# Kernel optimization log

Hardware: AMD Instinct MI355X
Metric: run time of the kernel (lower is better)

The kernel has to match this reference:

```python
import jax, jax.numpy as jnp
import numpy as np

N_NODES = 100000
N_EDGES = 1600000
N_GRAPHS = 512
EPS = 1e-12


def _glorot(key, shape):
    lim = float(np.sqrt(6.0 / (shape[0] + shape[1])))
    return jax.random.uniform(key, shape, jnp.float32, -lim, lim)


def setup_inputs() -> dict:
    key = jax.random.key(0)
    ks = jax.random.split(key, 16)
    x = jax.random.normal(ks[0], (N_NODES, 5), jnp.float32)
    edge_index = jax.random.randint(ks[1], (2, N_EDGES), 0, N_NODES)
    batch = jnp.sort(jax.random.randint(ks[2], (N_NODES,), 0, N_GRAPHS))
    return {
        "x": x,
        "edge_index": edge_index,
        "batch": batch,
        "num_graphs": N_GRAPHS,
        # pre: Linear(5, 32)
        "pre_w": _glorot(ks[3], (5, 32)), "pre_b": jnp.zeros((32,), jnp.float32),
        # conv1: SAGEConv(32, 64): lin_l (agg, bias), lin_r (root, no bias)
        "c1_wl": _glorot(ks[4], (32, 64)), "c1_bl": jnp.zeros((64,), jnp.float32),
        "c1_wr": _glorot(ks[5], (32, 64)),
        # conv2: SAGEConv(64, 64)
        "c2_wl": _glorot(ks[6], (64, 64)), "c2_bl": jnp.zeros((64,), jnp.float32),
        "c2_wr": _glorot(ks[7], (64, 64)),
        # post / out linears
        "p1_w": _glorot(ks[8], (64, 64)), "p1_b": jnp.zeros((64,), jnp.float32),
        "p2_w": _glorot(ks[9], (64, 16)), "p2_b": jnp.zeros((16,), jnp.float32),
        "o_w": _glorot(ks[10], (16, 1)), "o_b": jnp.zeros((1,), jnp.float32),
    }


def _sage_conv(x, src, dst, w_l, b_l, w_r, n_nodes):
    # mean-aggregate neighbor messages src -> dst
    msg = x[src]                                              # [E, d]
    agg = jax.ops.segment_sum(msg, dst, num_segments=n_nodes)  # [N, d]
    cnt = jax.ops.segment_sum(jnp.ones((src.shape[0], 1), x.dtype), dst,
                              num_segments=n_nodes)            # [N, 1]
    agg = jnp.where(cnt > 0, agg / jnp.maximum(cnt, 1.0), 0.0)
    out = agg @ w_l + b_l + x @ w_r
    # normalize=True -> L2 normalize per node
    nrm = jnp.linalg.norm(out, axis=-1, keepdims=True)
    return out / jnp.maximum(nrm, EPS)


def reference(x, edge_index, batch, num_graphs,
              pre_w, pre_b, c1_wl, c1_bl, c1_wr, c2_wl, c2_bl, c2_wr,
              p1_w, p1_b, p2_w, p2_b, o_w, o_b):
    n_nodes = x.shape[0]
    src, dst = edge_index[0], edge_index[1]
    h = jax.nn.relu(x @ pre_w + pre_b)
    h = jax.nn.relu(_sage_conv(h, src, dst, c1_wl, c1_bl, c1_wr, n_nodes))
    h = jax.nn.relu(_sage_conv(h, src, dst, c2_wl, c2_bl, c2_wr, n_nodes))
    # global mean pool over batch index
    s = jax.ops.segment_sum(h, batch, num_segments=num_graphs)          # [G, d]
    c = jax.ops.segment_sum(jnp.ones((n_nodes, 1), h.dtype), batch,
                            num_segments=num_graphs)                    # [G, 1]
    g = s / jnp.maximum(c, 1.0)
    g = jax.nn.relu(g @ p1_w + p1_b)
    g = jax.nn.relu(g @ p2_w + p2_b)
    out = g @ o_w + o_b
    return out.squeeze(-1)
```

## Files before the change

kernel.cpp:

```cpp
#include <hip/hip_runtime.h>

#define EPSN 1e-12f
#define TILE 2048
#define BSH 8
#define BNODES 256
#define SBMAX 512
#define BCAP 4608
#define CSRCAP 512

using frag_ab = __attribute__((ext_vector_type(8))) short;
using frag_cd = __attribute__((ext_vector_type(4))) float;
using f32x2   = __attribute__((ext_vector_type(2))) float;

template <bool B> struct BoolC { static constexpr bool value = B; };

__device__ inline unsigned short f2bf(float x) {
    union { float f; unsigned u; } v; v.f = x;
    unsigned r = v.u + 0x7fffu + ((v.u >> 16) & 1u);
    return (unsigned short)(r >> 16);
}
__device__ inline unsigned short pk2fp8(float a, float b) {
    return (unsigned short)(__builtin_amdgcn_cvt_pk_fp8_f32(a, b, 0, false) & 0xffff);
}
__device__ inline unsigned char to_fp8(float a) {
    return (unsigned char)(__builtin_amdgcn_cvt_pk_fp8_f32(a, a, 0, false) & 0xff);
}
__device__ inline void up8add(unsigned u, float* a) {
    f32x2 lo = __builtin_amdgcn_cvt_pk_f32_fp8(u, false);
    f32x2 hi = __builtin_amdgcn_cvt_pk_f32_fp8(u, true);
    a[0] += lo.x; a[1] += lo.y; a[2] += hi.x; a[3] += hi.y;
}

__global__ __launch_bounds__(256) void prep_all(
    const float* __restrict__ x, const float* __restrict__ pw,
    const float* __restrict__ pb, unsigned char* __restrict__ h0, int n,
    const float* __restrict__ w1l, const float* __restrict__ w1r,
    unsigned short* __restrict__ wpk1,
    const float* __restrict__ w2l, const float* __restrict__ w2r,
    unsigned short* __restrict__ wpk2,
    float* __restrict__ sg, int gtot,
    const int* __restrict__ dst, int* __restrict__ thistT, int e,
    int nsb, int nt) {
    __shared__ int lh[SBMAX];
    int tid = threadIdx.x;
    if (blockIdx.x < nt) {
        int b = blockIdx.x;
        for (int i = tid; i < nsb; i += 256) lh[i] = 0;
        __syncthreads();
        int base = b * TILE, lim = min(base + TILE, e);
        for (int i = base + tid; i < lim; i += 256) atomicAdd(&lh[dst[i] >> BSH], 1);
        __syncthreads();
        for (int i = tid; i < nsb; i += 256) thistT[(size_t)b * nsb + i] = lh[i];
        return;
    }
    int idx = (blockIdx.x - nt) * 256 + tid;
    int npre = n * 16;
    if (idx < npre) {
        int node = idx >> 4, j2 = idx & 15;
        int j = j2 * 2;
        float v0 = pb[j], v1 = pb[j + 1];
#pragma unroll
        for (int k = 0; k < 5; ++k) {
            float xv = x[node * 5 + k];
            v0 += xv * pw[k * 32 + j];
            v1 += xv * pw[k * 32 + j + 1];
        }
        ((unsigned short*)h0)[node * 16 + j2] =
            pk2fp8(fmaxf(v0, 0.f), fmaxf(v1, 0.f));
        return;
    }
    int o = idx - npre;
    if (o < 64 * 64) {
        int j = o / 64, k = o % 64;
        float v = (k < 32) ? w1l[k * 64 + j] : w1r[(k - 32) * 64 + j];
        wpk1[o] = f2bf(v);
        return;
    }
    o -= 64 * 64;
    if (o < 64 * 128) {
        int j = o / 128, k = o % 128;
        float v = (k < 64) ? w2l[k * 64 + j] : w2r[(k - 64) * 64 + j];
        wpk2[o] = f2bf(v);
        return;
    }
    o -= 64 * 128;
    if (o < gtot) sg[o] = 0.f;
}

__global__ __launch_bounds__(256) void tscan_k(const int* __restrict__ thistT,
                                               int* __restrict__ toffsT,
                                               int* __restrict__ btot,
                                               int nsb, int nt) {
    __shared__ int wsum[8];
    int b = blockIdx.x;
    int tid = threadIdx.x;
    int lane = tid & 63, w = tid >> 6;
    int run = 0;
    for (int base = 0; base < nt; base += 256) {
        int i = base + tid;
        int x = (i < nt) ? thistT[(size_t)i * nsb + b] : 0;
        int inc = x;
#pragma unroll
        for (int o = 1; o < 64; o <<= 1) {
            int t = __shfl_up(inc, o);
            if (lane >= o) inc += t;
        }
        if (lane == 63) wsum[w] = inc;
        __syncthreads();
        if (tid == 0) {
            int s = 0;
#pragma unroll
            for (int k = 0; k < 4; ++k) { int t = wsum[k]; wsum[k] = s; s += t; }
            wsum[4] = s;
        }
        __syncthreads();
        if (i < nt) toffsT[(size_t)b * nt + i] = inc - x + wsum[w] + run;
        run += wsum[4];
        __syncthreads();
    }
    if (tid == 0) btot[b] = run;
}

__global__ __launch_bounds__(256) void scat1_k(const int* __restrict__ src,
                                               const int* __restrict__ dst,
                                               const int* __restrict__ toffsT,
                                               int* __restrict__ staged, int e,
                                               int nsb, int nt) {
    __shared__ int cur[SBMAX];
    int tid = threadIdx.x;
    for (int i = tid; i < nsb; i += 256)
        cur[i] = i * BCAP + toffsT[(size_t)i * nt + blockIdx.x];
    __syncthreads();
    int base = blockIdx.x * TILE;
    int lim = min(base + TILE, e);
    for (int i = base + tid; i < lim; i += 256) {
        int d = dst[i];
        int p = atomicAdd(&cur[d >> BSH], 1);
        staged[p] = (src[i] << BSH) | (d & (BNODES - 1));
    }
}

__global__ __launch_bounds__(256) void scat2_k(const int* __restrict__ btot,
                                               const int* __restrict__ staged,
                                               int* __restrict__ csr,
                                               int* __restrict__ rofs,
                                               int* __restrict__ deg,
                                               int n, int nsb) {
    __shared__ int h[BNODES];
    __shared__ int cur[BNODES];
    __shared__ int wsum[8];
    int b = blockIdx.x;
    int tid = threadIdx.x;
    int lane = tid & 63, w = tid >> 6;
    int nlo = b << BSH;
    int nn = n - nlo; if (nn > BNODES) nn = BNODES;
    int lo = b * BCAP, hi = lo + btot[b];
    h[tid] = 0;
    __syncthreads();
    for (int i = lo + tid; i < hi; i += 256) atomicAdd(&h[staged[i] & (BNODES - 1)], 1);
    __syncthreads();
    int x = h[tid];
    int inc = x;
#pragma unroll
    for (int o = 1; o < 64; o <<= 1) {
        int t = __shfl_up(inc, o);
        if (lane >= o) inc += t;
    }
    if (lane == 63) wsum[w] = inc;
    __syncthreads();
    if (tid == 0) {
        int s = 0;
#pragma unroll
        for (int k = 0; k < 4; ++k) { int t = wsum[k]; wsum[k] = s; s += t; }
    }
    __syncthreads();
    int excl = inc - x + wsum[w];
    cur[tid] = excl;
    if (tid < nn) {
        rofs[nlo + tid] = lo + excl;
        deg[nlo + tid] = x;
    }
    __syncthreads();
    for (int i = lo + tid; i < hi; i += 256) {
        int v = staged[i];
        int p = atomicAdd(&cur[v & (BNODES - 1)], 1);
        csr[lo + p] = v >> BSH;
    }
}

template <int KE, bool POOL>
__global__ __launch_bounds__(256) void conv_mfma(
    const int* __restrict__ rofs, const int* __restrict__ deg,
    const int* __restrict__ csr,
    const unsigned char* __restrict__ hin, const unsigned short* __restrict__ wpk,
    const float* __restrict__ bl, const int* __restrict__ batch,
    float* __restrict__ sg, unsigned char* __restrict__ hout, int n) {
    constexpr int KT = 2 * KE;
    constexpr int ST = KT + 8;
    constexpr int KS = KT / 32;
    constexpr int LPE = KE / 4;
    constexpr int EPW = 64 / LPE;
    constexpr int RB = 16 / EPW;
    constexpr bool G4 = (LPE == 16);
    __shared__ unsigned short __attribute__((aligned(16))) Ab[16 * ST];
    __shared__ float __attribute__((aligned(16))) Nb[4][16];
    __shared__ int ro[16];
    __shared__ int dg[16];
    __shared__ int sb[16];
    __shared__ int csrL[CSRCAP];

    int tid = threadIdx.x;
    int w = tid >> 6;
    int lane = tid & 63;
    int quad = lane >> 4;
    int l16 = lane & 15;
    int base = blockIdx.x * 16;
    int ncol = w * 16 + l16;

    if (tid < 16) {
        int nd = base + tid;
        bool v = nd < n;
        ro[tid] = v ? rofs[nd] : 0;
        dg[tid] = v ? deg[nd] : 0;
        if (POOL) sb[tid] = v ? batch[nd] : -1;
    }

    frag_ab bfrag[KS];
#pragma unroll
    for (int s = 0; s < KS; ++s)
        bfrag[s] = *(const frag_ab*)&wpk[(((ncol * KS) + s) * 4 + quad) * 8];
    float bias = bl[ncol];
    __syncthreads();

    int ro0 = ro[0];
    int lastv = min(15, n - 1 - base);
    int span = ro[lastv] + dg[lastv] - ro0;
    int spanL = min(span, CSRCAP);
    for (int i = tid; i < spanL; i += 256) csrL[i] = csr[ro0 + i];

    int grp = lane / LPE;
    int p = lane % LPE;
    int beg[4], cnt[4];
#pragma unroll
    for (int i = 0; i < 4; ++i) {
        int li = w * 4 + i;
        beg[i] = ro[li] - ro0;
        cnt[i] = dg[li];
    }

    int sn = G4 ? grp : (grp & 3);
    bool doSelf = G4 || (grp >= 4);
    bool doAgg = G4 || (grp < 4);
    int snode = base + w * 4 + sn;
    unsigned selfv = 0u;
    if (doSelf && snode < n)
        selfv = *(const unsigned*)&hin[(size_t)snode * KE + p * 4];
    __syncthreads();

    float A[4][4] = {{0.f, 0.f, 0.f, 0.f}, {0.f, 0.f, 0.f, 0.f},
                     {0.f, 0.f, 0.f, 0.f}, {0.f, 0.f, 0.f, 0.f}};

    auto run_sweeps = [&](auto uselc) {
        constexpr bool USEL = decltype(uselc)::value;
        for (int s = 0;; ++s) {
            int e0 = s * 16;
            unsigned u[4][RB];
            bool act[4];
#pragma unroll
            for (int i = 0; i < 4; ++i) {
                act[i] = e0 < cnt[i];
                if (act[i]) {
#pragma unroll
                    for (int r = 0; r < RB; ++r) {
                        int ee = e0 + r * EPW + grp;
                        int cl = (ee < cnt[i]) ? ee : (cnt[i] - 1);
                        int off = beg[i] + cl;
                        int idx;
                        if (USEL || off < CSRCAP) idx = csrL[off];
                        else idx = csr[ro0 + off];
                        u[i][r] = *(const unsigned*)&hin[(size_t)idx * KE + p * 4];
                    }
                }
            }
#pragma unroll
            for (int i = 0; i < 4; ++i) {
                if (act[i]) {
#pragma unroll
                    for (int r = 0; r < RB; ++r)
                        if (e0 + r * EPW + grp < cnt[i]) up8add(u[i][r], A[i]);
                }
            }
            bool more = false;
#pragma unroll
            for (int i = 0; i < 4; ++i) more |= (e0 + 16) < cnt[i];
            if (!more) break;
        }
    };
    if (span <= CSRCAP) run_sweeps(BoolC<true>{});
    else run_sweeps(BoolC<false>{});

#pragma unroll
    for (int i = 0; i < 4; ++i) {
#pragma unroll
        for (int o = LPE; o < 64; o <<= 1) {
#pragma unroll
            for (int q = 0; q < 4; ++q) A[i][q] += __shfl_xor(A[i][q], o);
        }
    }

    float av0 = A[0][0], av1 = A[0][1], av2 = A[0][2], av3 = A[0][3];
    int cs = cnt[0];
#pragma unroll
    for (int i = 1; i < 4; ++i) {
        bool m = (sn == i);
        av0 = m ? A[i][0] : av0; av1 = m ? A[i][1] : av1;
        av2 = m ? A[i][2] : av2; av3 = m ? A[i][3] : av3;
        cs = m ? cnt[i] : cs;
    }
    {
        int li = w * 4 + sn;
        int node = base + li;
        if (node < n) {
            if (doAgg) {
                float inv = (cs > 0) ? 1.0f / (float)cs : 0.0f;
                uint2 o2;
                o2.x = (unsigned)f2bf(av0 * inv) | ((unsigned)f2bf(av1 * inv) << 16);
                o2.y = (unsigned)f2bf(av2 * inv) | ((unsigned)f2bf(av3 * inv) << 16);
                *(uint2*)&Ab[li * ST + p * 4] = o2;
            }
            if (doSelf) {
                f32x2 lo = __builtin_amdgcn_cvt_pk_f32_fp8(selfv, false);
                f32x2 hi = __builtin_amdgcn_cvt_pk_f32_fp8(selfv, true);
                uint2 o2;
                o2.x = (unsigned)f2bf(lo.x) | ((unsigned)f2bf(lo.y) << 16);
                o2.y = (unsigned)f2bf(hi.x) | ((unsigned)f2bf(hi.y) << 16);
                *(uint2*)&Ab[li * ST + KE + p * 4] = o2;
            }
        }
    }
    __syncthreads();

    frag_cd acc = (frag_cd){0.f, 0.f, 0.f, 0.f};
#pragma unroll
    for (int s = 0; s < KS; ++s) {
        frag_ab af = *(frag_ab*)&Ab[l16 * ST + s * 32 + quad * 8];
        acc = __builtin_amdgcn_mfma_f32_16x16x32_bf16(af, bfrag[s], acc, 0, 0, 0);
    }

    float vv[4], q[4];
#pragma unroll
    for (int i = 0; i < 4; ++i) {
        float v = acc[i] + bias;
        vv[i] = v;
        q[i] = v * v;
    }
#pragma unroll
    for (int o = 1; o < 16; o <<= 1) {
#pragma unroll
        for (int i = 0; i < 4; ++i) q[i] += __shfl_xor(q[i], o);
    }
    if (l16 == 0)
        *(float4*)&Nb[w][quad * 4] = make_float4(q[0], q[1], q[2], q[3]);
    __syncthreads();

    float s0 = 0.f, s1 = 0.f, s2 = 0.f, s3 = 0.f;
#pragma unroll
    for (int ww = 0; ww < 4; ++ww) {
        float4 xq = *(const float4*)&Nb[ww][quad * 4];
        s0 += xq.x; s1 += xq.y; s2 += xq.z; s3 += xq.w;
    }
    float ss[4] = {s0, s1, s2, s3};
    float pv[4];
#pragma unroll
    for (int i = 0; i < 4; ++i) {
        float nv = fmaxf(sqrtf(ss[i]), EPSN);
        pv[i] = fmaxf(vv[i] / nv, 0.f);
    }

    if (!POOL) {
#pragma unroll
        for (int i = 0; i < 4; ++i) {
            int node = base + quad * 4 + i;
            if (node < n)
                hout[(size_t)node * 64 + ncol] = to_fp8(pv[i]);
        }
    } else {
        int g0 = sb[0];
        int g1 = sb[min(15, n - 1 - base)];
        for (int g = g0; g <= g1; ++g) {
            float s = 0.f;
#pragma unroll
            for (int i = 0; i < 4; ++i)
                if (sb[quad * 4 + i] == g) s += pv[i];
            s += __shfl_xor(s, 16);
            s += __shfl_xor(s, 32);
            if (quad == 0) atomicAdd(&sg[(size_t)g * 64 + ncol], s);
        }
    }
}

__global__ __launch_bounds__(64) void mlp_k(
    const float* __restrict__ sg, const int* __restrict__ batch, int n,
    const float* __restrict__ p1w, const float* __restrict__ p1b,
    const float* __restrict__ p2w, const float* __restrict__ p2b,
    const float* __restrict__ ow, const float* __restrict__ ob,
    float* __restrict__ out) {
    __shared__ float gmean[64];
    __shared__ float a1[64];
    __shared__ float a2[16];
    int g = blockIdx.x;
    int j = threadIdx.x;
    int lo = 0, hi = n;
    while (lo < hi) { int m = (lo + hi) >> 1; if (batch[m] < g) lo = m + 1; else hi = m; }
    int start = lo;
    hi = n;
    while (lo < hi) { int m = (lo + hi) >> 1; if (batch[m] < g + 1) lo = m + 1; else hi = m; }
    float c = (float)(lo - start);
    gmean[j] = sg[(size_t)g * 64 + j] / fmaxf(c, 1.0f);
    __syncthreads();
    float v = p1b[j];
#pragma unroll 8
    for (int k = 0; k < 64; ++k) v = fmaf(gmean[k], p1w[k * 64 + j], v);
    a1[j] = fmaxf(v, 0.f);
    __syncthreads();
    if (j < 16) {
        float v2 = p2b[j];
#pragma unroll 8
        for (int k = 0; k < 64; ++k) v2 = fmaf(a1[k], p2w[k * 16 + j], v2);
        a2[j] = fmaxf(v2, 0.f);
    }
    __syncthreads();
    if (j == 0) {
        float v3 = ob[0];
#pragma unroll
        for (int k = 0; k < 16; ++k) v3 = fmaf(a2[k], ow[k], v3);
        out[g] = v3;
    }
}

extern "C" void kernel_launch(void* const* d_in, const int* in_sizes, int n_in,
                              void* d_out, int out_size, void* d_ws, size_t ws_size,
                              hipStream_t stream) {
    const float* x     = (const float*)d_in[0];
    const int*   ei    = (const int*)d_in[1];
    const int*   batch = (const int*)d_in[2];
    const float* pre_w = (const float*)d_in[4];
    const float* pre_b = (const float*)d_in[5];
    const float* c1_wl = (const float*)d_in[6];
    const float* c1_bl = (const float*)d_in[7];
    const float* c1_wr = (const float*)d_in[8];
    const float* c2_wl = (const float*)d_in[9];
    const float* c2_bl = (const float*)d_in[10];
    const float* c2_wr = (const float*)d_in[11];
    const float* p1w   = (const float*)d_in[12];
    const float* p1b   = (const float*)d_in[13];
    const float* p2w   = (const float*)d_in[14];
    const float* p2b   = (const float*)d_in[15];
    const float* ow    = (const float*)d_in[16];
    const float* ob    = (const float*)d_in[17];

    const int N = in_sizes[0] / 5;
    const int E = in_sizes[1] / 2;
    const int G = out_size;
    const int NT = (E + TILE - 1) / TILE;
    const int NSB = (N + BNODES - 1) / BNODES;
    const int* src = ei;
    const int* dst = ei + E;

    unsigned char* h0u = (unsigned char*)d_ws;
    unsigned char* h1u = h0u + (size_t)N * 32;
    unsigned short* wpk1 = (unsigned short*)(h1u + (size_t)N * 64);
    unsigned short* wpk2 = wpk1 + 64 * 64;
    float* sg    = (float*)(wpk2 + 64 * 128);
    int* rofs    = (int*)(sg + (size_t)G * 64);
    int* deg     = rofs + N;
    int* btot    = deg + N;
    int* thistT  = btot + NSB;
    int* toffsT  = thistT + (size_t)NT * NSB;
    int* staged  = toffsT + (size_t)NSB * NT;
    int* csr     = staged + (size_t)NSB * BCAP;

    int prep_tot = N * 16 + 64 * 64 + 64 * 128 + G * 64;
    int prep_blocks = (prep_tot + 255) / 256;
    prep_all<<<NT + prep_blocks, 256, 0, stream>>>(
        x, pre_w, pre_b, h0u, N, c1_wl, c1_wr, wpk1, c2_wl, c2_wr, wpk2,
        sg, G * 64, dst, thistT, E, NSB, NT);

    tscan_k<<<NSB, 256, 0, stream>>>(thistT, toffsT, btot, NSB, NT);
    scat1_k<<<NT, 256, 0, stream>>>(src, dst, toffsT, staged, E, NSB, NT);
    scat2_k<<<NSB, 256, 0, stream>>>(btot, staged, csr, rofs, deg, N, NSB);

    conv_mfma<32, false><<<(N + 15) / 16, 256, 0, stream>>>(
        rofs, deg, csr, h0u, wpk1, c1_bl, batch, sg, h1u, N);
    conv_mfma<64, true><<<(N + 15) / 16, 256, 0, stream>>>(
        rofs, deg, csr, h1u, wpk2, c2_bl, batch, sg, nullptr, N);

    mlp_k<<<G, 64, 0, stream>>>(sg, batch, N, p1w, p1b, p2w, p2b, ow, ob,
                                (float*)d_out);
}
```

Measured before the change: 236.5 us.

## Pad CSR rows to multiples of 16 with a zero sentinel node

```diff
diff --git a/kernel.cpp b/kernel.cpp
--- a/kernel.cpp
+++ b/kernel.cpp
@@ -6,7 +6,8 @@
 #define BNODES 256
 #define SBMAX 512
 #define BCAP 4608
-#define CSRCAP 512
+#define CSRBCAP 7168
+#define CSRCAP 768
 
 using frag_ab = __attribute__((ext_vector_type(8))) short;
 using frag_cd = __attribute__((ext_vector_type(4))) float;
@@ -25,15 +26,11 @@
 __device__ inline unsigned char to_fp8(float a) {
     return (unsigned char)(__builtin_amdgcn_cvt_pk_fp8_f32(a, a, 0, false) & 0xff);
 }
-__device__ inline void up8add(unsigned u, float* a) {
-    f32x2 lo = __builtin_amdgcn_cvt_pk_f32_fp8(u, false);
-    f32x2 hi = __builtin_amdgcn_cvt_pk_f32_fp8(u, true);
-    a[0] += lo.x; a[1] += lo.y; a[2] += hi.x; a[3] += hi.y;
-}
 
 __global__ __launch_bounds__(256) void prep_all(
     const float* __restrict__ x, const float* __restrict__ pw,
-    const float* __restrict__ pb, unsigned char* __restrict__ h0, int n,
+    const float* __restrict__ pb, unsigned char* __restrict__ h0,
+    unsigned char* __restrict__ h1, int n,
     const float* __restrict__ w1l, const float* __restrict__ w1r,
     unsigned short* __restrict__ wpk1,
     const float* __restrict__ w2l, const float* __restrict__ w2r,
@@ -84,7 +81,11 @@
         return;
     }
     o -= 64 * 128;
-    if (o < gtot) sg[o] = 0.f;
+    if (o < gtot) { sg[o] = 0.f; return; }
+    o -= gtot;
+    if (o < 8) { ((unsigned*)(h0 + (size_t)n * 32))[o] = 0u; return; }
+    o -= 8;
+    if (o < 16) ((unsigned*)(h1 + (size_t)n * 64))[o] = 0u;
 }
 
 __global__ __launch_bounds__(256) void tscan_k(const int* __restrict__ thistT,
@@ -154,13 +155,16 @@
     int lane = tid & 63, w = tid >> 6;
     int nlo = b << BSH;
     int nn = n - nlo; if (nn > BNODES) nn = BNODES;
-    int lo = b * BCAP, hi = lo + btot[b];
+    int lo_s = b * BCAP, hi_s = lo_s + btot[b];
+    int lo_c = b * CSRBCAP;
     h[tid] = 0;
     __syncthreads();
-    for (int i = lo + tid; i < hi; i += 256) atomicAdd(&h[staged[i] & (BNODES - 1)], 1);
+    for (int i = lo_s + tid; i < hi_s; i += 256)
+        atomicAdd(&h[staged[i] & (BNODES - 1)], 1);
     __syncthreads();
     int x = h[tid];
-    int inc = x;
+    int px = (x + 15) & ~15;
+    int inc = px;
 #pragma unroll
     for (int o = 1; o < 64; o <<= 1) {
         int t = __shfl_up(inc, o);
@@ -174,17 +178,18 @@
         for (int k = 0; k < 4; ++k) { int t = wsum[k]; wsum[k] = s; s += t; }
     }
     __syncthreads();
-    int excl = inc - x + wsum[w];
-    cur[tid] = excl;
+    int pexcl = inc - px + wsum[w];
+    cur[tid] = pexcl;
     if (tid < nn) {
-        rofs[nlo + tid] = lo + excl;
+        rofs[nlo + tid] = lo_c + pexcl;
         deg[nlo + tid] = x;
     }
-    __syncthreads();
-    for (int i = lo + tid; i < hi; i += 256) {
+    for (int k = x; k < px; ++k) csr[lo_c + pexcl + k] = n;
+    __syncthreads();
+    for (int i = lo_s + tid; i < hi_s; i += 256) {
         int v = staged[i];
         int p = atomicAdd(&cur[v & (BNODES - 1)], 1);
-        csr[lo + p] = v >> BSH;
+        csr[lo_c + p] = v >> BSH;
     }
 }
 
@@ -234,19 +239,21 @@
 
     int ro0 = ro[0];
     int lastv = min(15, n - 1 - base);
-    int span = ro[lastv] + dg[lastv] - ro0;
+    int span = ro[lastv] + ((dg[lastv] + 15) & ~15) - ro0;
     int spanL = min(span, CSRCAP);
     for (int i = tid; i < spanL; i += 256) csrL[i] = csr[ro0 + i];
 
     int grp = lane / LPE;
     int p = lane % LPE;
-    int beg[4], cnt[4];
+    int beg[4], cnt[4], pcnt[4];
 #pragma unroll
     for (int i = 0; i < 4; ++i) {
         int li = w * 4 + i;
         beg[i] = ro[li] - ro0;
         cnt[i] = dg[li];
-    }
+        pcnt[i] = (cnt[i] + 15) & ~15;
+    }
+    int msE = max(max(pcnt[0], pcnt[1]), max(pcnt[2], pcnt[3]));
 
     int sn = G4 ? grp : (grp & 3);
     bool doSelf = G4 || (grp >= 4);
@@ -257,24 +264,22 @@
         selfv = *(const unsigned*)&hin[(size_t)snode * KE + p * 4];
     __syncthreads();
 
-    float A[4][4] = {{0.f, 0.f, 0.f, 0.f}, {0.f, 0.f, 0.f, 0.f},
-                     {0.f, 0.f, 0.f, 0.f}, {0.f, 0.f, 0.f, 0.f}};
+    f32x2 AL[4][2];
+#pragma unroll
+    for (int i = 0; i < 4; ++i) { AL[i][0] = (f32x2){0.f, 0.f}; AL[i][1] = (f32x2){0.f, 0.f}; }
 
     auto run_sweeps = [&](auto uselc) {
         constexpr bool USEL = decltype(uselc)::value;
-        for (int s = 0;; ++s) {
-            int e0 = s * 16;
+        for (int e0 = 0; e0 < msE; e0 += 16) {
             unsigned u[4][RB];
             bool act[4];
 #pragma unroll
             for (int i = 0; i < 4; ++i) {
-                act[i] = e0 < cnt[i];
+                act[i] = e0 < pcnt[i];
                 if (act[i]) {
 #pragma unroll
                     for (int r = 0; r < RB; ++r) {
-                        int ee = e0 + r * EPW + grp;
-                        int cl = (ee < cnt[i]) ? ee : (cnt[i] - 1);
-                        int off = beg[i] + cl;
+                        int off = beg[i] + e0 + r * EPW + grp;
                         int idx;
                         if (USEL || off < CSRCAP) idx = csrL[off];
                         else idx = csr[ro0 + off];
@@ -286,18 +291,23 @@
             for (int i = 0; i < 4; ++i) {
                 if (act[i]) {
 #pragma unroll
-                    for (int r = 0; r < RB; ++r)
-                        if (e0 + r * EPW + grp < cnt[i]) up8add(u[i][r], A[i]);
+                    for (int r = 0; r < RB; ++r) {
+                        AL[i][0] += __builtin_amdgcn_cvt_pk_f32_fp8(u[i][r], false);
+                        AL[i][1] += __builtin_amdgcn_cvt_pk_f32_fp8(u[i][r], true);
+                    }
                 }
             }
-            bool more = false;
-#pragma unroll
-            for (int i = 0; i < 4; ++i) more |= (e0 + 16) < cnt[i];
-            if (!more) break;
         }
     };
     if (span <= CSRCAP) run_sweeps(BoolC<true>{});
     else run_sweeps(BoolC<false>{});
+
+    float A[4][4];
+#pragma unroll
+    for (int i = 0; i < 4; ++i) {
+        A[i][0] = AL[i][0].x; A[i][1] = AL[i][0].y;
+        A[i][2] = AL[i][1].x; A[i][3] = AL[i][1].y;
+    }
 
 #pragma unroll
     for (int i = 0; i < 4; ++i) {
@@ -468,8 +478,8 @@
     const int* dst = ei + E;
 
     unsigned char* h0u = (unsigned char*)d_ws;
-    unsigned char* h1u = h0u + (size_t)N * 32;
-    unsigned short* wpk1 = (unsigned short*)(h1u + (size_t)N * 64);
+    unsigned char* h1u = h0u + (size_t)(N + 1) * 32;
+    unsigned short* wpk1 = (unsigned short*)(h1u + (size_t)(N + 1) * 64);
     unsigned short* wpk2 = wpk1 + 64 * 64;
     float* sg    = (float*)(wpk2 + 64 * 128);
     int* rofs    = (int*)(sg + (size_t)G * 64);
@@ -480,10 +490,10 @@
     int* staged  = toffsT + (size_t)NSB * NT;
     int* csr     = staged + (size_t)NSB * BCAP;
 
-    int prep_tot = N * 16 + 64 * 64 + 64 * 128 + G * 64;
+    int prep_tot = N * 16 + 64 * 64 + 64 * 128 + G * 64 + 24;
     int prep_blocks = (prep_tot + 255) / 256;
     prep_all<<<NT + prep_blocks, 256, 0, stream>>>(
-        x, pre_w, pre_b, h0u, N, c1_wl, c1_wr, wpk1, c2_wl, c2_wr, wpk2,
+        x, pre_w, pre_b, h0u, h1u, N, c1_wl, c1_wr, wpk1, c2_wl, c2_wr, wpk2,
         sg, G * 64, dst, thistT, E, NSB, NT);
 
     tscan_k<<<NSB, 256, 0, stream>>>(thistT, toffsT, btot, NSB, NT);
```

Measured after the change: 246.2 us. 4.1% more time.

## Replace per-tile histogram scan with global atomic bucket reservation

Applied to the files above, without the earlier changes.

```diff
diff --git a/kernel.cpp b/kernel.cpp
--- a/kernel.cpp
+++ b/kernel.cpp
@@ -39,21 +39,8 @@
     const float* __restrict__ w2l, const float* __restrict__ w2r,
     unsigned short* __restrict__ wpk2,
     float* __restrict__ sg, int gtot,
-    const int* __restrict__ dst, int* __restrict__ thistT, int e,
-    int nsb, int nt) {
-    __shared__ int lh[SBMAX];
-    int tid = threadIdx.x;
-    if (blockIdx.x < nt) {
-        int b = blockIdx.x;
-        for (int i = tid; i < nsb; i += 256) lh[i] = 0;
-        __syncthreads();
-        int base = b * TILE, lim = min(base + TILE, e);
-        for (int i = base + tid; i < lim; i += 256) atomicAdd(&lh[dst[i] >> BSH], 1);
-        __syncthreads();
-        for (int i = tid; i < nsb; i += 256) thistT[(size_t)b * nsb + i] = lh[i];
-        return;
-    }
-    int idx = (blockIdx.x - nt) * 256 + tid;
+    int* __restrict__ bcnt, int nsb) {
+    int idx = blockIdx.x * 256 + threadIdx.x;
     int npre = n * 16;
     if (idx < npre) {
         int node = idx >> 4, j2 = idx & 15;
@@ -84,55 +71,32 @@
         return;
     }
     o -= 64 * 128;
-    if (o < gtot) sg[o] = 0.f;
-}
-
-__global__ __launch_bounds__(256) void tscan_k(const int* __restrict__ thistT,
-                                               int* __restrict__ toffsT,
-                                               int* __restrict__ btot,
-                                               int nsb, int nt) {
-    __shared__ int wsum[8];
-    int b = blockIdx.x;
-    int tid = threadIdx.x;
-    int lane = tid & 63, w = tid >> 6;
-    int run = 0;
-    for (int base = 0; base < nt; base += 256) {
-        int i = base + tid;
-        int x = (i < nt) ? thistT[(size_t)i * nsb + b] : 0;
-        int inc = x;
-#pragma unroll
-        for (int o = 1; o < 64; o <<= 1) {
-            int t = __shfl_up(inc, o);
-            if (lane >= o) inc += t;
-        }
-        if (lane == 63) wsum[w] = inc;
-        __syncthreads();
-        if (tid == 0) {
-            int s = 0;
-#pragma unroll
-            for (int k = 0; k < 4; ++k) { int t = wsum[k]; wsum[k] = s; s += t; }
-            wsum[4] = s;
-        }
-        __syncthreads();
-        if (i < nt) toffsT[(size_t)b * nt + i] = inc - x + wsum[w] + run;
-        run += wsum[4];
-        __syncthreads();
-    }
-    if (tid == 0) btot[b] = run;
+    if (o < gtot) { sg[o] = 0.f; return; }
+    o -= gtot;
+    if (o < nsb) bcnt[o] = 0;
 }
 
 __global__ __launch_bounds__(256) void scat1_k(const int* __restrict__ src,
                                                const int* __restrict__ dst,
-                                               const int* __restrict__ toffsT,
+                                               int* __restrict__ bcnt,
                                                int* __restrict__ staged, int e,
-                                               int nsb, int nt) {
+                                               int nsb) {
+    __shared__ int lh[SBMAX];
     __shared__ int cur[SBMAX];
     int tid = threadIdx.x;
-    for (int i = tid; i < nsb; i += 256)
-        cur[i] = i * BCAP + toffsT[(size_t)i * nt + blockIdx.x];
+    for (int i = tid; i < nsb; i += 256) lh[i] = 0;
     __syncthreads();
     int base = blockIdx.x * TILE;
     int lim = min(base + TILE, e);
+    for (int i = base + tid; i < lim; i += 256) atomicAdd(&lh[dst[i] >> BSH], 1);
+    __syncthreads();
+    for (int i = tid; i < nsb; i += 256) {
+        int c = lh[i];
+        int b = 0;
+        if (c) b = atomicAdd(&bcnt[i], c);
+        cur[i] = i * BCAP + b;
+    }
+    __syncthreads();
     for (int i = base + tid; i < lim; i += 256) {
         int d = dst[i];
         int p = atomicAdd(&cur[d >> BSH], 1);
@@ -467,28 +431,27 @@
     const int* src = ei;
     const int* dst = ei + E;
 
+    size_t h0_bytes = (((size_t)N * 32) + 127) & ~(size_t)127;
+    size_t h1_bytes = (((size_t)N * 64) + 127) & ~(size_t)127;
     unsigned char* h0u = (unsigned char*)d_ws;
-    unsigned char* h1u = h0u + (size_t)N * 32;
-    unsigned short* wpk1 = (unsigned short*)(h1u + (size_t)N * 64);
+    unsigned char* h1u = h0u + h0_bytes;
+    unsigned short* wpk1 = (unsigned short*)(h1u + h1_bytes);
     unsigned short* wpk2 = wpk1 + 64 * 64;
     float* sg    = (float*)(wpk2 + 64 * 128);
     int* rofs    = (int*)(sg + (size_t)G * 64);
     int* deg     = rofs + N;
-    int* btot    = deg + N;
-    int* thistT  = btot + NSB;
-    int* toffsT  = thistT + (size_t)NT * NSB;
-    int* staged  = toffsT + (size_t)NSB * NT;
+    int* bcnt    = deg + N;
+    int* staged  = bcnt + NSB;
     int* csr     = staged + (size_t)NSB * BCAP;
 
-    int prep_tot = N * 16 + 64 * 64 + 64 * 128 + G * 64;
+    int prep_tot = N * 16 + 64 * 64 + 64 * 128 + G * 64 + NSB;
     int prep_blocks = (prep_tot + 255) / 256;
-    prep_all<<<NT + prep_blocks, 256, 0, stream>>>(
+    prep_all<<<prep_blocks, 256, 0, stream>>>(
         x, pre_w, pre_b, h0u, N, c1_wl, c1_wr, wpk1, c2_wl, c2_wr, wpk2,
-        sg, G * 64, dst, thistT, E, NSB, NT);
-
-    tscan_k<<<NSB, 256, 0, stream>>>(thistT, toffsT, btot, NSB, NT);
-    scat1_k<<<NT, 256, 0, stream>>>(src, dst, toffsT, staged, E, NSB, NT);
-    scat2_k<<<NSB, 256, 0, stream>>>(btot, staged, csr, rofs, deg, N, NSB);
+        sg, G * 64, bcnt, NSB);
+
+    scat1_k<<<NT, 256, 0, stream>>>(src, dst, bcnt, staged, E, NSB);
+    scat2_k<<<NSB, 256, 0, stream>>>(bcnt, staged, csr, rofs, deg, N, NSB);
 
     conv_mfma<32, false><<<(N + 15) / 16, 256, 0, stream>>>(
         rofs, deg, csr, h0u, wpk1, c1_bl, batch, sg, h1u, N);
```

Result: slower. 241.8 us (+2.2%).
